# Performance work log

Hardware: AMD Instinct MI355X
Metric: run time of the kernel (lower is better)

Reference implementation:

```python
import jax, jax.numpy as jnp
import numpy as np

B, F, K, D = 512, 2048, 64, 16


def setup_inputs() -> dict:
    key = jax.random.key(0)
    k1, k2 = jax.random.split(key)
    x = jax.random.normal(k1, (B, F), dtype=jnp.float32)
    # glorot-uniform-ish init for the projection kernel [F, K, D]
    limit = np.sqrt(6.0 / (F + K * D)).astype(np.float32)
    kernel = jax.random.uniform(k2, (F, K, D), dtype=jnp.float32, minval=-limit, maxval=limit)
    return {"x": x, "kernel": kernel}


def reference(x, kernel):
    # activation: [B, K, D]
    act = jnp.einsum('bf,fkd->bkd', x, kernel)
    # pairwise L1 distance over D: diffs [B, K, D, B] -> abs_diffs [B, K, B]
    diffs = act[:, :, :, None] - jnp.transpose(act, (1, 2, 0))[None, :, :, :]
    abs_diffs = jnp.sum(jnp.abs(diffs), axis=2)
    # exp-similarity summed over the other batch elements (includes self: +1)
    feats = jnp.sum(jnp.exp(-abs_diffs), axis=2)  # [B, K]
    return jnp.concatenate([x, feats], axis=1)  # [B, F + K]
```

## Files before the change

### kernel.cpp

```cpp
#include <hip/hip_runtime.h>

#define B_   512
#define F_   2048
#define K_   64
#define D_   16
#define N_   1024
#define OUTW (F_+K_)

typedef __attribute__((ext_vector_type(8))) short short8;
typedef __attribute__((ext_vector_type(4))) float f32x4;

__device__ __forceinline__ ushort f2bf(float f) {
    union { float f; unsigned u; } un; un.f = f;
    unsigned u = un.u;
    u += 0x7FFF + ((u >> 16) & 1);
    return (ushort)(u >> 16);
}

__global__ __launch_bounds__(256) void convert_x_kernel(const float* __restrict__ x,
                                                        float* __restrict__ out,
                                                        ushort* __restrict__ xb) {
    const int i = blockIdx.x * 256 + threadIdx.x;
    float4 v = ((const float4*)x)[i];
    const int b = i >> 9, c = i & 511;
    ((float4*)out)[b * (OUTW / 4) + c] = v;
    ushort4 u = make_ushort4(f2bf(v.x), f2bf(v.y), f2bf(v.z), f2bf(v.w));
    ((ushort4*)xb)[i] = u;
}

__global__ __launch_bounds__(256) void convert_wt_kernel(const float* __restrict__ w,
                                                         ushort* __restrict__ wt) {
    __shared__ float t[32][33];
    const int f0 = blockIdx.x * 32;
    const int n0 = blockIdx.y * 32;
    const int tid = threadIdx.x;
    const int r = tid >> 3;
    const int c4 = (tid & 7) * 4;
    float4 v = *(const float4*)(w + (size_t)(f0 + r) * N_ + n0 + c4);
    t[r][c4 + 0] = v.x; t[r][c4 + 1] = v.y; t[r][c4 + 2] = v.z; t[r][c4 + 3] = v.w;
    __syncthreads();
    ushort4 u = make_ushort4(f2bf(t[c4 + 0][r]), f2bf(t[c4 + 1][r]),
                             f2bf(t[c4 + 2][r]), f2bf(t[c4 + 3][r]));
    *(ushort4*)(wt + (size_t)(n0 + r) * F_ + f0 + c4) = u;
}

#define KSPLIT 4
#define KCH (F_/KSPLIT)

__global__ __launch_bounds__(256) void gemm_mfma_kernel(const ushort* __restrict__ xb,
                                                        const ushort* __restrict__ wt,
                                                        float* __restrict__ act) {
    const int bm0 = blockIdx.x * 64;
    const int bn0 = blockIdx.y * 64;
    const int f0  = blockIdx.z * KCH;

    const int tid = threadIdx.x;
    const int l   = tid & 63;
    const int w   = tid >> 6;
    const int mw  = (w >> 1) * 32;
    const int nw  = (w & 1) * 32;
    const int lr  = l & 15;
    const int lk  = (l >> 4) * 8;

    const ushort* pa0 = xb + (size_t)(bm0 + mw + lr) * F_ + f0 + lk;
    const ushort* pa1 = pa0 + 16 * F_;
    const ushort* pb0 = wt + (size_t)(bn0 + nw + lr) * F_ + f0 + lk;
    const ushort* pb1 = pb0 + 16 * F_;

    f32x4 acc00 = {}, acc01 = {}, acc10 = {}, acc11 = {};

    #pragma unroll 4
    for (int kk = 0; kk < KCH; kk += 32) {
        short8 a0 = *(const short8*)(pa0 + kk);
        short8 a1 = *(const short8*)(pa1 + kk);
        short8 b0 = *(const short8*)(pb0 + kk);
        short8 b1 = *(const short8*)(pb1 + kk);
        acc00 = __builtin_amdgcn_mfma_f32_16x16x32_bf16(a0, b0, acc00, 0, 0, 0);
        acc01 = __builtin_amdgcn_mfma_f32_16x16x32_bf16(a0, b1, acc01, 0, 0, 0);
        acc10 = __builtin_amdgcn_mfma_f32_16x16x32_bf16(a1, b0, acc10, 0, 0, 0);
        acc11 = __builtin_amdgcn_mfma_f32_16x16x32_bf16(a1, b1, acc11, 0, 0, 0);
    }

    const int mbase = bm0 + mw + (l >> 4) * 4;
    #pragma unroll
    for (int j = 0; j < 2; ++j) {
        const int n = bn0 + nw + j * 16 + lr;
        const int k = n >> 4, d = n & 15;
        float* dst = act + (size_t)k * (B_ * D_) + d;
        const f32x4 c0 = j ? acc01 : acc00;
        const f32x4 c1 = j ? acc11 : acc10;
        #pragma unroll
        for (int r = 0; r < 4; ++r) {
            atomicAdd(dst + (size_t)(mbase + r) * D_,      c0[r]);
            atomicAdd(dst + (size_t)(mbase + 16 + r) * D_, c1[r]);
        }
    }
}

__global__ __launch_bounds__(256) void pairwise_kernel(const float* __restrict__ act,
                                                       float* __restrict__ out) {
    __shared__ float s_act[B_ * D_];
    __shared__ float red[4][64];

    const int bt = blockIdx.x;
    const int k  = blockIdx.y;
    const int tid  = threadIdx.x;
    const int lane = tid & 63;
    const int wave = tid >> 6;

    const float4* src = (const float4*)(act + (size_t)k * B_ * D_);
    #pragma unroll
    for (int i = tid; i < (B_ * D_) / 4; i += 256)
        ((float4*)s_act)[i] = src[i];
    __syncthreads();

    const int b = bt * 64 + lane;
    float a[D_];
    #pragma unroll
    for (int d = 0; d < D_; ++d) a[d] = s_act[b * D_ + d];

    float p = 0.0f;
    const int b2lo = wave * 128;
    #pragma unroll 4
    for (int b2 = b2lo; b2 < b2lo + 128; ++b2) {
        const float* v = &s_act[b2 * D_];
        float dist = 0.0f;
        #pragma unroll
        for (int d = 0; d < D_; ++d) dist += fabsf(a[d] - v[d]);
        p += __expf(-dist);
    }

    red[wave][lane] = p;
    __syncthreads();
    if (wave == 0) {
        const float total = red[0][lane] + red[1][lane] + red[2][lane] + red[3][lane];
        out[(size_t)b * OUTW + F_ + k] = total;
    }
}

extern "C" void kernel_launch(void* const* d_in, const int* in_sizes, int n_in,
                              void* d_out, int out_size, void* d_ws, size_t ws_size,
                              hipStream_t stream) {
    const float* x = (const float*)d_in[0];
    const float* wsrc = (const float*)d_in[1];
    float* out = (float*)d_out;

    ushort* xb  = (ushort*)d_ws;
    ushort* wt  = (ushort*)((char*)d_ws + (size_t)2 * 1024 * 1024);
    float*  act = (float*)((char*)d_ws + (size_t)6 * 1024 * 1024);

    hipMemsetAsync(act, 0, (size_t)K_ * B_ * D_ * sizeof(float), stream);
    convert_x_kernel<<<1024, 256, 0, stream>>>(x, out, xb);
    convert_wt_kernel<<<dim3(64, 32), 256, 0, stream>>>(wsrc, wt);
    gemm_mfma_kernel<<<dim3(8, 16, KSPLIT), 256, 0, stream>>>(xb, wt, act);
    pairwise_kernel<<<dim3(8, K_), 256, 0, stream>>>(act, out);
}
```

Measured before the change: 107.7 us.

## Drop split-K atomics, fold log2e into x, use raw exp2, widen pairwise blocks

The GEMM no longer splits K four ways with atomicAdd into a zeroed buffer. Each block now covers a 64x32 tile over the full F and stores its results directly, which also removes the memset. The log2(e) factor is folded into x during bf16 conversion, so the pairwise kernel can call v_exp_f32 through inline asm instead of __expf. The pairwise kernel also moves to 512 threads with float4 LDS reads and two accumulators, at the cost of fewer GEMM blocks, longer per-block K loops, and extra rounding from the pre-scaled bf16 values.

```diff
diff --git a/kernel.cpp b/kernel.cpp
--- a/kernel.cpp
+++ b/kernel.cpp
@@ -6,6 +6,7 @@
 #define D_   16
 #define N_   1024
 #define OUTW (F_+K_)
+#define LOG2E 1.44269504088896340736f
 
 typedef __attribute__((ext_vector_type(8))) short short8;
 typedef __attribute__((ext_vector_type(4))) float f32x4;
@@ -17,6 +18,12 @@
     return (ushort)(u >> 16);
 }
 
+__device__ __forceinline__ float exp2_neg(float x) {
+    float r;
+    asm("v_exp_f32 %0, -%1" : "=v"(r) : "v"(x));
+    return r;
+}
+
 __global__ __launch_bounds__(256) void convert_x_kernel(const float* __restrict__ x,
                                                         float* __restrict__ out,
                                                         ushort* __restrict__ xb) {
@@ -24,7 +31,8 @@
     float4 v = ((const float4*)x)[i];
     const int b = i >> 9, c = i & 511;
     ((float4*)out)[b * (OUTW / 4) + c] = v;
-    ushort4 u = make_ushort4(f2bf(v.x), f2bf(v.y), f2bf(v.z), f2bf(v.w));
+    ushort4 u = make_ushort4(f2bf(v.x * LOG2E), f2bf(v.y * LOG2E),
+                             f2bf(v.z * LOG2E), f2bf(v.w * LOG2E));
     ((ushort4*)xb)[i] = u;
 }
 
@@ -44,63 +52,49 @@
     *(ushort4*)(wt + (size_t)(n0 + r) * F_ + f0 + c4) = u;
 }
 
-#define KSPLIT 4
-#define KCH (F_/KSPLIT)
-
 __global__ __launch_bounds__(256) void gemm_mfma_kernel(const ushort* __restrict__ xb,
                                                         const ushort* __restrict__ wt,
                                                         float* __restrict__ act) {
     const int bm0 = blockIdx.x * 64;
-    const int bn0 = blockIdx.y * 64;
-    const int f0  = blockIdx.z * KCH;
-
+    const int bn0 = blockIdx.y * 32;
     const int tid = threadIdx.x;
     const int l   = tid & 63;
     const int w   = tid >> 6;
     const int mw  = (w >> 1) * 32;
-    const int nw  = (w & 1) * 32;
+    const int nw  = (w & 1) * 16;
     const int lr  = l & 15;
     const int lk  = (l >> 4) * 8;
 
-    const ushort* pa0 = xb + (size_t)(bm0 + mw + lr) * F_ + f0 + lk;
+    const ushort* pa0 = xb + (size_t)(bm0 + mw + lr) * F_ + lk;
     const ushort* pa1 = pa0 + 16 * F_;
-    const ushort* pb0 = wt + (size_t)(bn0 + nw + lr) * F_ + f0 + lk;
-    const ushort* pb1 = pb0 + 16 * F_;
+    const ushort* pb0 = wt + (size_t)(bn0 + nw + lr) * F_ + lk;
 
-    f32x4 acc00 = {}, acc01 = {}, acc10 = {}, acc11 = {};
+    f32x4 acc0 = {}, acc1 = {};
 
     #pragma unroll 4
-    for (int kk = 0; kk < KCH; kk += 32) {
+    for (int kk = 0; kk < F_; kk += 32) {
         short8 a0 = *(const short8*)(pa0 + kk);
         short8 a1 = *(const short8*)(pa1 + kk);
         short8 b0 = *(const short8*)(pb0 + kk);
-        short8 b1 = *(const short8*)(pb1 + kk);
-        acc00 = __builtin_amdgcn_mfma_f32_16x16x32_bf16(a0, b0, acc00, 0, 0, 0);
-        acc01 = __builtin_amdgcn_mfma_f32_16x16x32_bf16(a0, b1, acc01, 0, 0, 0);
-        acc10 = __builtin_amdgcn_mfma_f32_16x16x32_bf16(a1, b0, acc10, 0, 0, 0);
-        acc11 = __builtin_amdgcn_mfma_f32_16x16x32_bf16(a1, b1, acc11, 0, 0, 0);
+        acc0 = __builtin_amdgcn_mfma_f32_16x16x32_bf16(a0, b0, acc0, 0, 0, 0);
+        acc1 = __builtin_amdgcn_mfma_f32_16x16x32_bf16(a1, b0, acc1, 0, 0, 0);
     }
 
+    const int n = bn0 + nw + lr;
+    const int k = n >> 4, d = n & 15;
     const int mbase = bm0 + mw + (l >> 4) * 4;
+    float* dst = act + (size_t)k * (B_ * D_) + d;
     #pragma unroll
-    for (int j = 0; j < 2; ++j) {
-        const int n = bn0 + nw + j * 16 + lr;
-        const int k = n >> 4, d = n & 15;
-        float* dst = act + (size_t)k * (B_ * D_) + d;
-        const f32x4 c0 = j ? acc01 : acc00;
-        const f32x4 c1 = j ? acc11 : acc10;
-        #pragma unroll
-        for (int r = 0; r < 4; ++r) {
-            atomicAdd(dst + (size_t)(mbase + r) * D_,      c0[r]);
-            atomicAdd(dst + (size_t)(mbase + 16 + r) * D_, c1[r]);
-        }
+    for (int r = 0; r < 4; ++r) {
+        dst[(size_t)(mbase + r) * D_]      = acc0[r];
+        dst[(size_t)(mbase + 16 + r) * D_] = acc1[r];
     }
 }
 
-__global__ __launch_bounds__(256) void pairwise_kernel(const float* __restrict__ act,
+__global__ __launch_bounds__(512) void pairwise_kernel(const float* __restrict__ act,
                                                        float* __restrict__ out) {
     __shared__ float s_act[B_ * D_];
-    __shared__ float red[4][64];
+    __shared__ float red[8][64];
 
     const int bt = blockIdx.x;
     const int k  = blockIdx.y;
@@ -108,32 +102,56 @@
     const int lane = tid & 63;
     const int wave = tid >> 6;
 
-    const float4* src = (const float4*)(act + (size_t)k * B_ * D_);
+    const float4* src = (const float4*)(act + (size_t)k * (B_ * D_));
     #pragma unroll
-    for (int i = tid; i < (B_ * D_) / 4; i += 256)
-        ((float4*)s_act)[i] = src[i];
+    for (int i = 0; i < 4; ++i)
+        ((float4*)s_act)[tid + i * 512] = src[tid + i * 512];
     __syncthreads();
 
     const int b = bt * 64 + lane;
-    float a[D_];
-    #pragma unroll
-    for (int d = 0; d < D_; ++d) a[d] = s_act[b * D_ + d];
+    const float4* arow = (const float4*)&s_act[b * D_];
+    const float4 a0 = arow[0], a1 = arow[1], a2 = arow[2], a3 = arow[3];
 
-    float p = 0.0f;
-    const int b2lo = wave * 128;
-    #pragma unroll 4
-    for (int b2 = b2lo; b2 < b2lo + 128; ++b2) {
-        const float* v = &s_act[b2 * D_];
-        float dist = 0.0f;
-        #pragma unroll
-        for (int d = 0; d < D_; ++d) dist += fabsf(a[d] - v[d]);
-        p += __expf(-dist);
+    float p0 = 0.0f, p1 = 0.0f;
+    const int b2lo = wave * 64;
+    #pragma unroll 2
+    for (int b2 = b2lo; b2 < b2lo + 64; b2 += 2) {
+        {
+            const float4* v = (const float4*)&s_act[b2 * D_];
+            const float4 v0 = v[0], v1 = v[1], v2 = v[2], v3 = v[3];
+            float t0 = fabsf(a0.x - v0.x) + fabsf(a0.y - v0.y);
+            float t1 = fabsf(a0.z - v0.z) + fabsf(a0.w - v0.w);
+            float t2 = fabsf(a1.x - v1.x) + fabsf(a1.y - v1.y);
+            float t3 = fabsf(a1.z - v1.z) + fabsf(a1.w - v1.w);
+            float t4 = fabsf(a2.x - v2.x) + fabsf(a2.y - v2.y);
+            float t5 = fabsf(a2.z - v2.z) + fabsf(a2.w - v2.w);
+            float t6 = fabsf(a3.x - v3.x) + fabsf(a3.y - v3.y);
+            float t7 = fabsf(a3.z - v3.z) + fabsf(a3.w - v3.w);
+            float s = ((t0 + t1) + (t2 + t3)) + ((t4 + t5) + (t6 + t7));
+            p0 += exp2_neg(s);
+        }
+        {
+            const float4* v = (const float4*)&s_act[(b2 + 1) * D_];
+            const float4 v0 = v[0], v1 = v[1], v2 = v[2], v3 = v[3];
+            float t0 = fabsf(a0.x - v0.x) + fabsf(a0.y - v0.y);
+            float t1 = fabsf(a0.z - v0.z) + fabsf(a0.w - v0.w);
+            float t2 = fabsf(a1.x - v1.x) + fabsf(a1.y - v1.y);
+            float t3 = fabsf(a1.z - v1.z) + fabsf(a1.w - v1.w);
+            float t4 = fabsf(a2.x - v2.x) + fabsf(a2.y - v2.y);
+            float t5 = fabsf(a2.z - v2.z) + fabsf(a2.w - v2.w);
+            float t6 = fabsf(a3.x - v3.x) + fabsf(a3.y - v3.y);
+            float t7 = fabsf(a3.z - v3.z) + fabsf(a3.w - v3.w);
+            float s = ((t0 + t1) + (t2 + t3)) + ((t4 + t5) + (t6 + t7));
+            p1 += exp2_neg(s);
+        }
     }
 
-    red[wave][lane] = p;
+    red[wave][lane] = p0 + p1;
     __syncthreads();
     if (wave == 0) {
-        const float total = red[0][lane] + red[1][lane] + red[2][lane] + red[3][lane];
+        float total = 0.0f;
+        #pragma unroll
+        for (int i = 0; i < 8; ++i) total += red[i][lane];
         out[(size_t)b * OUTW + F_ + k] = total;
     }
 }
@@ -149,9 +167,8 @@
     ushort* wt  = (ushort*)((char*)d_ws + (size_t)2 * 1024 * 1024);
     float*  act = (float*)((char*)d_ws + (size_t)6 * 1024 * 1024);
 
-    hipMemsetAsync(act, 0, (size_t)K_ * B_ * D_ * sizeof(float), stream);
     convert_x_kernel<<<1024, 256, 0, stream>>>(x, out, xb);
     convert_wt_kernel<<<dim3(64, 32), 256, 0, stream>>>(wsrc, wt);
-    gemm_mfma_kernel<<<dim3(8, 16, KSPLIT), 256, 0, stream>>>(xb, wt, act);
-    pairwise_kernel<<<dim3(8, K_), 256, 0, stream>>>(act, out);
+    gemm_mfma_kernel<<<dim3(8, 32), 256, 0, stream>>>(xb, wt, act);
+    pairwise_kernel<<<dim3(8, K_), 512, 0, stream>>>(act, out);
 }
```

After: 112.5 us. +4.4%, slower.
